# Optimization experiments

Measured on AMD Instinct MI355X. Metric: run time of the kernel, lower is better.

## Reference

```python
import jax, jax.numpy as jnp
import numpy as np

B, L, S, H, E = 4, 2048, 2048, 8, 64

def setup_inputs() -> dict:
    key = jax.random.key(0)
    kq, kk, kv, kt, kd = jax.random.split(key, 5)
    return {
        "queries": jax.random.normal(kq, (B, L, H, E), dtype=jnp.float32),
        "keys": jax.random.normal(kk, (B, S, H, E), dtype=jnp.float32),
        "values": jax.random.normal(kv, (B, S, H, E), dtype=jnp.float32),
        "attn_mask": jnp.zeros((1,), dtype=bool),
        "tau": jax.random.uniform(kt, (B, 1), dtype=jnp.float32),
        "delta": jax.random.normal(kd, (B, 1), dtype=jnp.float32),
    }

def reference(queries, keys, values, attn_mask, tau, delta):
    # queries: [B,L,H,E], keys: [B,S,H,E], values: [B,S,H,D]
    Bq, Lq, Hq, Eq = queries.shape
    scale = 1.0 / jnp.sqrt(jnp.float32(Eq))
    scores = jnp.einsum('blhe,bshe->bhls', queries, keys)  # [B,H,L,S]
    scores = scores * tau.reshape(Bq, 1, 1, 1)             # per-batch tau scale
    scores = scores + delta.reshape(Bq, 1, 1, 1)           # per-batch delta bias
    A = jax.nn.softmax(scale * scores, axis=-1)            # dropout is identity at eval
    V = jnp.einsum('bhls,bshd->blhd', A, values)           # [B,L,H,D]
    return V
```

## Files before the change

### kernel.cpp

```cpp
#include <hip/hip_runtime.h>
#include <hip/hip_bf16.h>
#include <stdint.h>

#define LL 2048
#define SS 2048
#define HH 8
#define EE 64
#define RSG 512

typedef float v4f  __attribute__((ext_vector_type(4)));
typedef float v16f __attribute__((ext_vector_type(16)));
typedef short s4v  __attribute__((ext_vector_type(4)));
typedef short s8v  __attribute__((ext_vector_type(8)));

__device__ __forceinline__ short f2bf(float f) {
    unsigned u = __float_as_uint(f);
    u = (u + 0x7fffu + ((u >> 16) & 1u)) >> 16;
    return (short)u;
}

__device__ __forceinline__ s4v pack4bf(float a, float b, float c, float d) {
    float2 ab = make_float2(a, b), cd = make_float2(c, d);
    __hip_bfloat162 r0 = __float22bfloat162_rn(ab);
    __hip_bfloat162 r1 = __float22bfloat162_rn(cd);
    s4v r;
    __builtin_memcpy(&r, &r0, 4);
    __builtin_memcpy(((char*)&r) + 4, &r1, 4);
    return r;
}

__global__ __launch_bounds__(256)
void dsattn_prep(const float* __restrict__ kk, const float* __restrict__ vv,
                 short* __restrict__ kimg, short* __restrict__ vimg)
{
    __shared__ float T[64][68];
    const int t = threadIdx.x;
    const int blk = blockIdx.x;
    if (blk < 1024) {
        const int vb = blk;
        const int b = vb >> 8, h = (vb >> 5) & 7, ts = vb & 31;
        const float* kp = kk + ((size_t)b * SS + ts * 64) * RSG + h * EE;
        #pragma unroll
        for (int c = 0; c < 4; ++c) {
            int idx = c * 256 + t, s = idx >> 4, e0 = (idx & 15) << 2;
            *(v4f*)&T[s][e0] = *(const v4f*)(kp + (size_t)s * RSG + e0);
        }
        __syncthreads();
        short* dst = kimg + (size_t)vb * 4096;
        #pragma unroll
        for (int half = 0; half < 2; ++half) {
            int ci = half * 256 + t;
            int echunk = ci >> 6, srow = ci & 63;
            s8v ov;
            #pragma unroll
            for (int j = 0; j < 8; ++j) ov[j] = f2bf(T[srow][echunk * 8 + j]);
            *(s8v*)(dst + ci * 8) = ov;
        }
    } else {
        const int vb = blk - 1024;
        const int b = vb >> 8, h = (vb >> 5) & 7, ts = vb & 31;
        const float* vp = vv + ((size_t)b * SS + ts * 64) * RSG + h * EE;
        #pragma unroll
        for (int c = 0; c < 4; ++c) {
            int idx = c * 256 + t, s = idx >> 4, e0 = (idx & 15) << 2;
            *(v4f*)&T[s][e0] = *(const v4f*)(vp + (size_t)s * RSG + e0);
        }
        __syncthreads();
        short* dst = vimg + (size_t)vb * 4096;
        #pragma unroll
        for (int half = 0; half < 2; ++half) {
            int ci = half * 256 + t;
            int c = ci >> 6, e = ci & 63;
            int sbase = 16 * (c >> 1) + 4 * (c & 1);
            s8v ov;
            #pragma unroll
            for (int j = 0; j < 8; ++j) {
                int s = sbase + 8 * (j >> 2) + (j & 3);
                ov[j] = f2bf(T[s][e]);
            }
            *(s8v*)(dst + ci * 8) = ov;
        }
    }
}

__global__ __launch_bounds__(256, 2)
void dsattn_main(const float* __restrict__ q, const short* __restrict__ kimg,
                 const short* __restrict__ vimg, const float* __restrict__ tau,
                 float* __restrict__ out)
{
    __shared__ short KV[4][8192];

    const int t    = threadIdx.x;
    const int lane = t & 63;
    const int w    = t >> 6;
    const int l31  = lane & 31;
    const int hi   = lane >> 5;

    const int hw = blockIdx.x;
    const int wu = (hw & 7) * 64 + (hw >> 3);
    const int mt = wu & 15;
    const int h  = (wu >> 4) & 7;
    const int b  = wu >> 7;

    const float scf = 0.125f * 1.44269504088896f * tau[b];

    s8v qf[4];
    {
        const float* qb = q + ((size_t)b * LL + (size_t)mt * 128 + w * 32 + l31) * RSG
                            + h * EE + 8 * hi;
        #pragma unroll
        for (int ks = 0; ks < 4; ++ks) {
            v4f a0 = *(const v4f*)(qb + 16 * ks);
            v4f a1 = *(const v4f*)(qb + 16 * ks + 4);
            s4v p0 = pack4bf(a0[0] * scf, a0[1] * scf, a0[2] * scf, a0[3] * scf);
            s4v p1 = pack4bf(a1[0] * scf, a1[1] * scf, a1[2] * scf, a1[3] * scf);
            s8v f;
            #pragma unroll
            for (int j = 0; j < 4; ++j) { f[j] = p0[j]; f[4 + j] = p1[j]; }
            qf[ks] = f;
        }
    }

    const char* gsrc;
    {
        const size_t pan = (size_t)((b * 8 + h) * 32) * 8192;
        if (w < 2) gsrc = (const char*)kimg + pan + w * 4096 + lane * 16;
        else       gsrc = (const char*)vimg + pan + (w - 2) * 4096 + lane * 16;
    }

    #define STAGE(slot)                                                                   \
        {                                                                                 \
            _Pragma("unroll")                                                             \
            for (int j = 0; j < 4; ++j) {                                                 \
                __builtin_amdgcn_global_load_lds(                                         \
                    (const __attribute__((address_space(1))) unsigned*)(gsrc + j * 1024), \
                    (__attribute__((address_space(3))) unsigned*)&KV[slot][w * 2048 + j * 512], \
                    16, 0, 0);                                                            \
            }                                                                             \
            gsrc += 8192;                                                                 \
        }

    v16f oacc[2];
    #pragma unroll
    for (int mb = 0; mb < 2; ++mb)
        #pragma unroll
        for (int r = 0; r < 16; ++r) oacc[mb][r] = 0.0f;
    float rsum = 0.0f;

    const int rb = hi * 512 + l31 * 8;

    asm volatile("s_waitcnt vmcnt(0)" ::: "memory");
    __builtin_amdgcn_sched_barrier(0);
    STAGE(0);
    STAGE(1);
    STAGE(2);

    #pragma unroll 4
    for (int it = 0; it < 32; ++it) {
        const int p = it & 3;

        __builtin_amdgcn_sched_barrier(0);
        if (it <= 29)      asm volatile("s_waitcnt vmcnt(8)" ::: "memory");
        else if (it == 30) asm volatile("s_waitcnt vmcnt(4)" ::: "memory");
        else               asm volatile("s_waitcnt vmcnt(0)" ::: "memory");
        __builtin_amdgcn_s_barrier();
        __builtin_amdgcn_sched_barrier(0);

        if (it <= 28) STAGE((it + 3) & 3);

        const short* Kp = &KV[p][0];
        const short* Vp = &KV[p][4096];

        v16f st[2];
        #pragma unroll
        for (int mb = 0; mb < 2; ++mb) {
            v16f z;
            #pragma unroll
            for (int r = 0; r < 16; ++r) z[r] = 0.0f;
            #pragma unroll
            for (int ks = 0; ks < 4; ++ks) {
                s8v kf = *(const s8v*)&Kp[ks * 1024 + mb * 256 + rb];
                z = __builtin_amdgcn_mfma_f32_32x32x16_bf16(kf, qf[ks], z, 0, 0, 0);
            }
            st[mb] = z;
        }

        #pragma unroll
        for (int mb = 0; mb < 2; ++mb)
            #pragma unroll
            for (int r = 0; r < 16; ++r)
                st[mb][r] = __builtin_amdgcn_exp2f(st[mb][r]);
        float s0 = 0.f, s1 = 0.f;
        #pragma unroll
        for (int r = 0; r < 16; ++r) { s0 += st[0][r]; s1 += st[1][r]; }
        rsum += s0 + s1;

        s8v pf[4];
        #pragma unroll
        for (int tt = 0; tt < 4; ++tt) {
            int o = 8 * (tt & 1);
            const v16f& sv = st[tt >> 1];
            s4v lo = pack4bf(sv[o + 0], sv[o + 1], sv[o + 2], sv[o + 3]);
            s4v hs = pack4bf(sv[o + 4], sv[o + 5], sv[o + 6], sv[o + 7]);
            s8v f;
            #pragma unroll
            for (int j = 0; j < 4; ++j) { f[j] = lo[j]; f[4 + j] = hs[j]; }
            pf[tt] = f;
        }

        #pragma unroll
        for (int mb = 0; mb < 2; ++mb) {
            v16f acc = oacc[mb];
            #pragma unroll
            for (int ks = 0; ks < 4; ++ks) {
                s8v vf = *(const s8v*)&Vp[ks * 1024 + mb * 256 + rb];
                acc = __builtin_amdgcn_mfma_f32_32x32x16_bf16(vf, pf[ks], acc, 0, 0, 0);
            }
            oacc[mb] = acc;
        }
    }

    rsum += __shfl_xor(rsum, 32);
    const float inv = 1.0f / rsum;
    float* ob = out + ((size_t)b * LL + (size_t)mt * 128 + w * 32 + l31) * RSG + h * EE;
    #pragma unroll
    for (int mb = 0; mb < 2; ++mb)
        #pragma unroll
        for (int rq = 0; rq < 4; ++rq) {
            int e0 = 32 * mb + 8 * rq + 4 * hi;
            v4f o4 = { oacc[mb][4 * rq + 0] * inv, oacc[mb][4 * rq + 1] * inv,
                       oacc[mb][4 * rq + 2] * inv, oacc[mb][4 * rq + 3] * inv };
            *(v4f*)(ob + e0) = o4;
        }
}

extern "C" void kernel_launch(void* const* d_in, const int* in_sizes, int n_in,
                              void* d_out, int out_size, void* d_ws, size_t ws_size,
                              hipStream_t stream) {
    const float* q     = (const float*)d_in[0];
    const float* k     = (const float*)d_in[1];
    const float* v     = (const float*)d_in[2];
    const float* tau   = (const float*)d_in[4];
    float* out = (float*)d_out;

    short* kimg = (short*)d_ws;
    short* vimg = kimg + (size_t)4 * SS * RSG;

    dsattn_prep<<<dim3(2048), dim3(256), 0, stream>>>(k, v, kimg, vimg);
    dsattn_main<<<dim3(512), dim3(256), 0, stream>>>(q, kimg, vimg, tau, out);
}
```

Before: 136.2 us.

## Double-buffer two KV tiles per superstage instead of a 4-slot single-tile ring

Restructures the LDS pipeline from a 4-slot ring holding one 64-key tile per slot into 2 slots that each hold two tiles. Each loop iteration now computes two tiles between barriers and refills the slot it just used, which needs a second barrier per iteration before restaging. The aim is fewer waits and barriers per key processed and more MFMA work per synchronisation point. In exchange, prefetch depth drops from three tiles ahead to effectively one superstage ahead, the loop is no longer unrolled, and holding more live score registers may raise register pressure.

```diff
diff --git a/kernel.cpp b/kernel.cpp
--- a/kernel.cpp
+++ b/kernel.cpp
@@ -88,7 +88,7 @@
                  const short* __restrict__ vimg, const float* __restrict__ tau,
                  float* __restrict__ out)
 {
-    __shared__ short KV[4][8192];
+    __shared__ short KV[2][16384];
 
     const int t    = threadIdx.x;
     const int lane = t & 63;
@@ -128,7 +128,7 @@
         else       gsrc = (const char*)vimg + pan + (w - 2) * 4096 + lane * 16;
     }
 
-    #define STAGE(slot)                                                                   \
+    #define SUPERSTAGE(slot)                                                              \
         {                                                                                 \
             _Pragma("unroll")                                                             \
             for (int j = 0; j < 4; ++j) {                                                 \
@@ -137,7 +137,14 @@
                     (__attribute__((address_space(3))) unsigned*)&KV[slot][w * 2048 + j * 512], \
                     16, 0, 0);                                                            \
             }                                                                             \
-            gsrc += 8192;                                                                 \
+            _Pragma("unroll")                                                             \
+            for (int j = 0; j < 4; ++j) {                                                 \
+                __builtin_amdgcn_global_load_lds(                                         \
+                    (const __attribute__((address_space(1))) unsigned*)(gsrc + 8192 + j * 1024), \
+                    (__attribute__((address_space(3))) unsigned*)&KV[slot][8192 + w * 2048 + j * 512], \
+                    16, 0, 0);                                                            \
+            }                                                                             \
+            gsrc += 16384;                                                                \
         }
 
     v16f oacc[2];
@@ -151,72 +158,80 @@
 
     asm volatile("s_waitcnt vmcnt(0)" ::: "memory");
     __builtin_amdgcn_sched_barrier(0);
-    STAGE(0);
-    STAGE(1);
-    STAGE(2);
-
-    #pragma unroll 4
-    for (int it = 0; it < 32; ++it) {
-        const int p = it & 3;
+    SUPERSTAGE(0);
+    SUPERSTAGE(1);
+
+    #pragma unroll 1
+    for (int sw = 0; sw < 16; ++sw) {
+        const int p = sw & 1;
 
         __builtin_amdgcn_sched_barrier(0);
-        if (it <= 29)      asm volatile("s_waitcnt vmcnt(8)" ::: "memory");
-        else if (it == 30) asm volatile("s_waitcnt vmcnt(4)" ::: "memory");
-        else               asm volatile("s_waitcnt vmcnt(0)" ::: "memory");
+        if (sw <= 14) asm volatile("s_waitcnt vmcnt(8)" ::: "memory");
+        else          asm volatile("s_waitcnt vmcnt(0)" ::: "memory");
         __builtin_amdgcn_s_barrier();
         __builtin_amdgcn_sched_barrier(0);
 
-        if (it <= 28) STAGE((it + 3) & 3);
-
-        const short* Kp = &KV[p][0];
-        const short* Vp = &KV[p][4096];
-
-        v16f st[2];
-        #pragma unroll
-        for (int mb = 0; mb < 2; ++mb) {
-            v16f z;
-            #pragma unroll
-            for (int r = 0; r < 16; ++r) z[r] = 0.0f;
-            #pragma unroll
-            for (int ks = 0; ks < 4; ++ks) {
-                s8v kf = *(const s8v*)&Kp[ks * 1024 + mb * 256 + rb];
-                z = __builtin_amdgcn_mfma_f32_32x32x16_bf16(kf, qf[ks], z, 0, 0, 0);
-            }
-            st[mb] = z;
-        }
-
-        #pragma unroll
-        for (int mb = 0; mb < 2; ++mb)
-            #pragma unroll
-            for (int r = 0; r < 16; ++r)
-                st[mb][r] = __builtin_amdgcn_exp2f(st[mb][r]);
-        float s0 = 0.f, s1 = 0.f;
-        #pragma unroll
-        for (int r = 0; r < 16; ++r) { s0 += st[0][r]; s1 += st[1][r]; }
-        rsum += s0 + s1;
-
-        s8v pf[4];
-        #pragma unroll
-        for (int tt = 0; tt < 4; ++tt) {
-            int o = 8 * (tt & 1);
-            const v16f& sv = st[tt >> 1];
-            s4v lo = pack4bf(sv[o + 0], sv[o + 1], sv[o + 2], sv[o + 3]);
-            s4v hs = pack4bf(sv[o + 4], sv[o + 5], sv[o + 6], sv[o + 7]);
-            s8v f;
-            #pragma unroll
-            for (int j = 0; j < 4; ++j) { f[j] = lo[j]; f[4 + j] = hs[j]; }
-            pf[tt] = f;
-        }
-
-        #pragma unroll
-        for (int mb = 0; mb < 2; ++mb) {
-            v16f acc = oacc[mb];
-            #pragma unroll
-            for (int ks = 0; ks < 4; ++ks) {
-                s8v vf = *(const s8v*)&Vp[ks * 1024 + mb * 256 + rb];
-                acc = __builtin_amdgcn_mfma_f32_32x32x16_bf16(vf, pf[ks], acc, 0, 0, 0);
-            }
-            oacc[mb] = acc;
+        v16f st[2][2];
+        #pragma unroll
+        for (int tl = 0; tl < 2; ++tl) {
+            const short* Kp = &KV[p][tl * 8192];
+            #pragma unroll
+            for (int mb = 0; mb < 2; ++mb) {
+                v16f z;
+                #pragma unroll
+                for (int r = 0; r < 16; ++r) z[r] = 0.0f;
+                #pragma unroll
+                for (int ks = 0; ks < 4; ++ks) {
+                    s8v kf = *(const s8v*)&Kp[ks * 1024 + mb * 256 + rb];
+                    z = __builtin_amdgcn_mfma_f32_32x32x16_bf16(kf, qf[ks], z, 0, 0, 0);
+                }
+                st[tl][mb] = z;
+            }
+        }
+
+        #pragma unroll
+        for (int tl = 0; tl < 2; ++tl) {
+            #pragma unroll
+            for (int mb = 0; mb < 2; ++mb)
+                #pragma unroll
+                for (int r = 0; r < 16; ++r)
+                    st[tl][mb][r] = __builtin_amdgcn_exp2f(st[tl][mb][r]);
+            float s0 = 0.f, s1 = 0.f;
+            #pragma unroll
+            for (int r = 0; r < 16; ++r) { s0 += st[tl][0][r]; s1 += st[tl][1][r]; }
+            rsum += s0 + s1;
+
+            s8v pf[4];
+            #pragma unroll
+            for (int tt = 0; tt < 4; ++tt) {
+                int o = 8 * (tt & 1);
+                const v16f& sv = st[tl][tt >> 1];
+                s4v lo = pack4bf(sv[o + 0], sv[o + 1], sv[o + 2], sv[o + 3]);
+                s4v hs = pack4bf(sv[o + 4], sv[o + 5], sv[o + 6], sv[o + 7]);
+                s8v f;
+                #pragma unroll
+                for (int j = 0; j < 4; ++j) { f[j] = lo[j]; f[4 + j] = hs[j]; }
+                pf[tt] = f;
+            }
+
+            const short* Vp = &KV[p][tl * 8192 + 4096];
+            #pragma unroll
+            for (int mb = 0; mb < 2; ++mb) {
+                v16f acc = oacc[mb];
+                #pragma unroll
+                for (int ks = 0; ks < 4; ++ks) {
+                    s8v vf = *(const s8v*)&Vp[ks * 1024 + mb * 256 + rb];
+                    acc = __builtin_amdgcn_mfma_f32_32x32x16_bf16(vf, pf[ks], acc, 0, 0, 0);
+                }
+                oacc[mb] = acc;
+            }
+        }
+
+        if (sw <= 13) {
+            __builtin_amdgcn_sched_barrier(0);
+            __builtin_amdgcn_s_barrier();
+            __builtin_amdgcn_sched_barrier(0);
+            SUPERSTAGE(p);
         }
     }
 
```

Measured after the change: 134.2 us. Within noise of the previous version (-1.5%).

## Split key sequence across two wave groups per block and merge partial outputs

Applied to the files above, without the earlier changes.

Doubles the block to 512 threads. Two groups of four waves each process half of the key/value sequence, with their own double-buffered LDS slots. At the end, group 1 writes its partial output accumulators and row sums to shared memory and group 0 adds them before normalizing and storing. This is meant to raise the number of active waves per CU and hide latency, since 512 blocks alone cannot fill the GPU. In exchange, buffering drops from four stages to two, an extra barrier is added per iteration, and a reduction step through LDS is added at the end.

```diff
diff --git a/kernel.cpp b/kernel.cpp
--- a/kernel.cpp
+++ b/kernel.cpp
@@ -83,16 +83,18 @@
     }
 }
 
-__global__ __launch_bounds__(256, 2)
+__global__ __launch_bounds__(512, 4)
 void dsattn_main(const float* __restrict__ q, const short* __restrict__ kimg,
                  const short* __restrict__ vimg, const float* __restrict__ tau,
                  float* __restrict__ out)
 {
-    __shared__ short KV[4][8192];
+    __shared__ short KV[2][2][8192];
 
     const int t    = threadIdx.x;
     const int lane = t & 63;
     const int w    = t >> 6;
+    const int w4   = w & 3;
+    const int grp  = w >> 2;
     const int l31  = lane & 31;
     const int hi   = lane >> 5;
 
@@ -106,7 +108,7 @@
 
     s8v qf[4];
     {
-        const float* qb = q + ((size_t)b * LL + (size_t)mt * 128 + w * 32 + l31) * RSG
+        const float* qb = q + ((size_t)b * LL + (size_t)mt * 128 + w4 * 32 + l31) * RSG
                             + h * EE + 8 * hi;
         #pragma unroll
         for (int ks = 0; ks < 4; ++ks) {
@@ -123,9 +125,10 @@
 
     const char* gsrc;
     {
-        const size_t pan = (size_t)((b * 8 + h) * 32) * 8192;
-        if (w < 2) gsrc = (const char*)kimg + pan + w * 4096 + lane * 16;
-        else       gsrc = (const char*)vimg + pan + (w - 2) * 4096 + lane * 16;
+        const size_t pan  = (size_t)((b * 8 + h) * 32) * 8192;
+        const size_t soff = (size_t)grp * 16 * 8192;
+        if (w4 < 2) gsrc = (const char*)kimg + pan + soff + w4 * 4096 + lane * 16;
+        else        gsrc = (const char*)vimg + pan + soff + (w4 - 2) * 4096 + lane * 16;
     }
 
     #define STAGE(slot)                                                                   \
@@ -134,7 +137,7 @@
             for (int j = 0; j < 4; ++j) {                                                 \
                 __builtin_amdgcn_global_load_lds(                                         \
                     (const __attribute__((address_space(1))) unsigned*)(gsrc + j * 1024), \
-                    (__attribute__((address_space(3))) unsigned*)&KV[slot][w * 2048 + j * 512], \
+                    (__attribute__((address_space(3))) unsigned*)&KV[grp][slot][w4 * 2048 + j * 512], \
                     16, 0, 0);                                                            \
             }                                                                             \
             gsrc += 8192;                                                                 \
@@ -153,23 +156,19 @@
     __builtin_amdgcn_sched_barrier(0);
     STAGE(0);
     STAGE(1);
-    STAGE(2);
-
-    #pragma unroll 4
-    for (int it = 0; it < 32; ++it) {
-        const int p = it & 3;
+
+    #pragma unroll 1
+    for (int sw = 0; sw < 16; ++sw) {
+        const int p = sw & 1;
 
         __builtin_amdgcn_sched_barrier(0);
-        if (it <= 29)      asm volatile("s_waitcnt vmcnt(8)" ::: "memory");
-        else if (it == 30) asm volatile("s_waitcnt vmcnt(4)" ::: "memory");
-        else               asm volatile("s_waitcnt vmcnt(0)" ::: "memory");
+        if (sw <= 14) asm volatile("s_waitcnt vmcnt(4)" ::: "memory");
+        else          asm volatile("s_waitcnt vmcnt(0)" ::: "memory");
         __builtin_amdgcn_s_barrier();
         __builtin_amdgcn_sched_barrier(0);
 
-        if (it <= 28) STAGE((it + 3) & 3);
-
-        const short* Kp = &KV[p][0];
-        const short* Vp = &KV[p][4096];
+        const short* Kp = &KV[grp][p][0];
+        const short* Vp = &KV[grp][p][4096];
 
         v16f st[2];
         #pragma unroll
@@ -218,20 +217,45 @@
             }
             oacc[mb] = acc;
         }
-    }
-
-    rsum += __shfl_xor(rsum, 32);
-    const float inv = 1.0f / rsum;
-    float* ob = out + ((size_t)b * LL + (size_t)mt * 128 + w * 32 + l31) * RSG + h * EE;
-    #pragma unroll
-    for (int mb = 0; mb < 2; ++mb)
-        #pragma unroll
-        for (int rq = 0; rq < 4; ++rq) {
-            int e0 = 32 * mb + 8 * rq + 4 * hi;
-            v4f o4 = { oacc[mb][4 * rq + 0] * inv, oacc[mb][4 * rq + 1] * inv,
-                       oacc[mb][4 * rq + 2] * inv, oacc[mb][4 * rq + 3] * inv };
-            *(v4f*)(ob + e0) = o4;
-        }
+
+        if (sw <= 13) {
+            __builtin_amdgcn_sched_barrier(0);
+            __builtin_amdgcn_s_barrier();
+            __builtin_amdgcn_sched_barrier(0);
+            STAGE(p);
+        }
+    }
+
+    __syncthreads();
+    float* sh = (float*)&KV[0][0][0];
+    const int slot = (t & 255) * 33;
+    if (grp == 1) {
+        #pragma unroll
+        for (int mb = 0; mb < 2; ++mb)
+            #pragma unroll
+            for (int r = 0; r < 16; ++r) sh[slot + mb * 16 + r] = oacc[mb][r];
+        sh[slot + 32] = rsum;
+    }
+    __syncthreads();
+    if (grp == 0) {
+        #pragma unroll
+        for (int mb = 0; mb < 2; ++mb)
+            #pragma unroll
+            for (int r = 0; r < 16; ++r) oacc[mb][r] += sh[slot + mb * 16 + r];
+        rsum += sh[slot + 32];
+        rsum += __shfl_xor(rsum, 32);
+        const float inv = 1.0f / rsum;
+        float* ob = out + ((size_t)b * LL + (size_t)mt * 128 + w4 * 32 + l31) * RSG + h * EE;
+        #pragma unroll
+        for (int mb = 0; mb < 2; ++mb)
+            #pragma unroll
+            for (int rq = 0; rq < 4; ++rq) {
+                int e0 = 32 * mb + 8 * rq + 4 * hi;
+                v4f o4 = { oacc[mb][4 * rq + 0] * inv, oacc[mb][4 * rq + 1] * inv,
+                           oacc[mb][4 * rq + 2] * inv, oacc[mb][4 * rq + 3] * inv };
+                *(v4f*)(ob + e0) = o4;
+            }
+    }
 }
 
 extern "C" void kernel_launch(void* const* d_in, const int* in_sizes, int n_in,
@@ -247,5 +271,5 @@
     short* vimg = kimg + (size_t)4 * SS * RSG;
 
     dsattn_prep<<<dim3(2048), dim3(256), 0, stream>>>(k, v, kimg, vimg);
-    dsattn_main<<<dim3(512), dim3(256), 0, stream>>>(q, kimg, vimg, tau, out);
-}
+    dsattn_main<<<dim3(512), dim3(512), 0, stream>>>(q, kimg, vimg, tau, out);
+}
```

Result: no change. 135.3 us (-0.7%).

## Restructure K/V prep to load full 512-wide rows and convert to bf16 early

Applied to the files above, without the earlier changes.

The prep kernel now gives each block 64 sequence rows across all 8 heads, split into two 32-row halves. Each half reads contiguous 2 KB rows, converts to bf16 while storing into shared memory, and then scatters per-head tiles into the K and V images. The goal is more coalesced global reads and half the shared-memory footprint per element. The cost is fewer blocks (256 instead of 2048), which lowers parallelism and latency hiding on a large GPU. The change also leaves a dead shared-memory load in the K path.

```diff
diff --git a/kernel.cpp b/kernel.cpp
--- a/kernel.cpp
+++ b/kernel.cpp
@@ -33,53 +33,55 @@
 void dsattn_prep(const float* __restrict__ kk, const float* __restrict__ vv,
                  short* __restrict__ kimg, short* __restrict__ vimg)
 {
-    __shared__ float T[64][68];
-    const int t = threadIdx.x;
+    __shared__ short T[32][520];
+    const int t   = threadIdx.x;
     const int blk = blockIdx.x;
-    if (blk < 1024) {
-        const int vb = blk;
-        const int b = vb >> 8, h = (vb >> 5) & 7, ts = vb & 31;
-        const float* kp = kk + ((size_t)b * SS + ts * 64) * RSG + h * EE;
-        #pragma unroll
-        for (int c = 0; c < 4; ++c) {
-            int idx = c * 256 + t, s = idx >> 4, e0 = (idx & 15) << 2;
-            *(v4f*)&T[s][e0] = *(const v4f*)(kp + (size_t)s * RSG + e0);
+    const int isV = blk >> 7;
+    const int b   = (blk & 127) >> 5;
+    const int ts  = blk & 31;
+    const float* src = (isV ? vv : kk) + ((size_t)b * SS + ts * 64) * RSG;
+    short* dimg = isV ? vimg : kimg;
+
+    #pragma unroll 1
+    for (int half = 0; half < 2; ++half) {
+        const float* hsrc = src + (size_t)(half * 32) * RSG;
+        #pragma unroll
+        for (int i = 0; i < 16; ++i) {
+            int g = i * 256 + t;
+            int row = g >> 7, c4 = (g & 127) << 2;
+            v4f d = *(const v4f*)(hsrc + (size_t)row * RSG + c4);
+            *(s4v*)&T[row][c4] = pack4bf(d[0], d[1], d[2], d[3]);
         }
         __syncthreads();
-        short* dst = kimg + (size_t)vb * 4096;
-        #pragma unroll
-        for (int half = 0; half < 2; ++half) {
-            int ci = half * 256 + t;
-            int echunk = ci >> 6, srow = ci & 63;
-            s8v ov;
-            #pragma unroll
-            for (int j = 0; j < 8; ++j) ov[j] = f2bf(T[srow][echunk * 8 + j]);
-            *(s8v*)(dst + ci * 8) = ov;
-        }
-    } else {
-        const int vb = blk - 1024;
-        const int b = vb >> 8, h = (vb >> 5) & 7, ts = vb & 31;
-        const float* vp = vv + ((size_t)b * SS + ts * 64) * RSG + h * EE;
-        #pragma unroll
-        for (int c = 0; c < 4; ++c) {
-            int idx = c * 256 + t, s = idx >> 4, e0 = (idx & 15) << 2;
-            *(v4f*)&T[s][e0] = *(const v4f*)(vp + (size_t)s * RSG + e0);
+
+        if (!isV) {
+            const int echunk = t >> 5, srow = t & 31;
+            const s8v kv = *(const s8v*)&T[srow][0 * 64 + echunk * 8];
+            (void)kv;
+            #pragma unroll
+            for (int h = 0; h < 8; ++h) {
+                s8v ov = *(const s8v*)&T[srow][h * 64 + echunk * 8];
+                short* dst = dimg + ((size_t)((b * 8 + h) * 32 + ts)) * 4096
+                           + (echunk * 64 + half * 32 + srow) * 8;
+                *(s8v*)dst = ov;
+            }
+        } else {
+            const int c = (t >> 6) + half * 4, e = t & 63;
+            const int sbase = 16 * (c >> 1) + 4 * (c & 1) - half * 32;
+            #pragma unroll
+            for (int h = 0; h < 8; ++h) {
+                s8v ov;
+                #pragma unroll
+                for (int j = 0; j < 8; ++j) {
+                    int s = sbase + 8 * (j >> 2) + (j & 3);
+                    ov[j] = T[s][h * 64 + e];
+                }
+                short* dst = dimg + ((size_t)((b * 8 + h) * 32 + ts)) * 4096
+                           + (c * 64 + e) * 8;
+                *(s8v*)dst = ov;
+            }
         }
         __syncthreads();
-        short* dst = vimg + (size_t)vb * 4096;
-        #pragma unroll
-        for (int half = 0; half < 2; ++half) {
-            int ci = half * 256 + t;
-            int c = ci >> 6, e = ci & 63;
-            int sbase = 16 * (c >> 1) + 4 * (c & 1);
-            s8v ov;
-            #pragma unroll
-            for (int j = 0; j < 8; ++j) {
-                int s = sbase + 8 * (j >> 2) + (j & 3);
-                ov[j] = f2bf(T[s][e]);
-            }
-            *(s8v*)(dst + ci * 8) = ov;
-        }
     }
 }
 
@@ -246,6 +248,6 @@
     short* kimg = (short*)d_ws;
     short* vimg = kimg + (size_t)4 * SS * RSG;
 
-    dsattn_prep<<<dim3(2048), dim3(256), 0, stream>>>(k, v, kimg, vimg);
+    dsattn_prep<<<dim3(256), dim3(256), 0, stream>>>(k, v, kimg, vimg);
     dsattn_main<<<dim3(512), dim3(256), 0, stream>>>(q, kimg, vimg, tau, out);
 }
```

Measured after the change: 135.6 us. About the same (-0.4%).
